# Kernel tuning notes

Measured on AMD Instinct MI355X. Metric: run time of the kernel, lower is better.

The kernel has to match this reference:

```python
import jax, jax.numpy as jnp
import numpy as np

B, S, D = 2, 2048, 2048
H, KVH, DH = 16, 4, 128
WIN = 128
THETA = 10000.0  # local rope (layer_idx=0 -> local/sliding path)


def setup_inputs() -> dict:
    key = jax.random.key(0)
    ks = jax.random.split(key, 5)
    return {
        "x": jax.random.normal(ks[0], (B, S, D), dtype=jnp.float32),
        "Wq": jax.random.normal(ks[1], (H * DH, D), dtype=jnp.float32) * 0.02,
        "Wk": jax.random.normal(ks[2], (KVH * DH, D), dtype=jnp.float32) * 0.02,
        "Wv": jax.random.normal(ks[3], (KVH * DH, D), dtype=jnp.float32) * 0.02,
        "Wo": jax.random.normal(ks[4], (D, H * DH), dtype=jnp.float32) * 0.02,
    }


def _rotate_half(t):
    half = t.shape[-1] // 2
    return jnp.concatenate([-t[..., half:], t[..., :half]], axis=-1)


def _rope_tables(seq_len, head_dim, theta, dtype):
    inv_freq = 1.0 / (theta ** (jnp.arange(0, head_dim, 2, dtype=jnp.float32) / head_dim))
    freqs = jnp.arange(seq_len, dtype=jnp.float32)[:, None] * inv_freq[None, :]  # [S, DH/2]
    # source does repeat_interleave(cos, 2, dim=-1): [S, DH]
    cos = jnp.repeat(jnp.cos(freqs), 2, axis=-1).astype(dtype)
    sin = jnp.repeat(jnp.sin(freqs), 2, axis=-1).astype(dtype)
    return cos[None, :, None, :], sin[None, :, None, :]  # broadcast over [B,S,H,DH]


def reference(x, Wq, Wk, Wv, Wo):
    b, s, _ = x.shape
    q = (x @ Wq.T).reshape(b, s, H, DH)
    k = (x @ Wk.T).reshape(b, s, KVH, DH)
    v = (x @ Wv.T).reshape(b, s, KVH, DH)

    cos, sin = _rope_tables(s, DH, THETA, x.dtype)
    q = q * cos + _rotate_half(q) * sin
    k = k * cos + _rotate_half(k) * sin

    # GQA: repeat_interleave kv heads to n_heads
    groups = H // KVH
    k = jnp.repeat(k, groups, axis=2)
    v = jnp.repeat(v, groups, axis=2)

    q = q.transpose(0, 2, 1, 3)  # [B,H,S,DH]
    k = k.transpose(0, 2, 1, 3)
    v = v.transpose(0, 2, 1, 3)

    scale = DH ** -0.5
    scores = jnp.einsum('bhqd,bhkd->bhqk', q, k) * scale  # [B,H,S,S]

    # faithful local mask from source: q_idx >= k_idx - window_size
    iq = jnp.arange(s)[:, None]
    ik = jnp.arange(s)[None, :]
    mask = iq >= (ik - WIN)  # [S,S]
    scores = jnp.where(mask[None, None, :, :], scores, jnp.float32(-jnp.inf).astype(scores.dtype))

    attn = jax.nn.softmax(scores, axis=-1)
    out = jnp.einsum('bhqk,bhkd->bhqd', attn, v)
    out = out.transpose(0, 2, 1, 3).reshape(b, s, H * DH)
    return out @ Wo.T
```

## Files before the change

### kernel.cpp

```cpp
#include <hip/hip_runtime.h>
#include <hip/hip_bf16.h>

using bf16 = __hip_bfloat16;
typedef __attribute__((ext_vector_type(8))) short short8;
typedef __attribute__((ext_vector_type(4))) float floatx4;

#define AS1 __attribute__((address_space(1)))
#define AS3 __attribute__((address_space(3)))

__device__ __forceinline__ floatx4 mfma16(short8 a, short8 b, floatx4 c) {
  return __builtin_amdgcn_mfma_f32_16x16x32_bf16(a, b, c, 0, 0, 0);
}
__device__ __forceinline__ void gload16(const bf16* g, bf16* l) {
  __builtin_amdgcn_global_load_lds((const AS1 unsigned*)g, (AS3 unsigned*)l, 16, 0, 0);
}

__global__ void cast_bf16_k(const float* __restrict__ src, bf16* __restrict__ dst, int n) {
  int i = (blockIdx.x * 256 + threadIdx.x) * 4;
  if (i >= n) return;
  float4 v = *(const float4*)(src + i);
  bf16 t[4] = {__float2bfloat16(v.x), __float2bfloat16(v.y),
               __float2bfloat16(v.z), __float2bfloat16(v.w)};
  *(ushort4*)(dst + i) = *(const ushort4*)t;
}

template <typename OutT>
__global__ __launch_bounds__(256, 2)
void gemm_bt(const bf16* __restrict__ A, const bf16* __restrict__ B,
             OutT* __restrict__ C, int M, int N, int K) {
  __shared__ alignas(16) bf16 As[128 * 32];
  __shared__ alignas(16) bf16 Bs[128 * 32];
  const int tid = threadIdx.x;
  const int w = tid >> 6, lane = tid & 63, l16 = lane & 15, quad = lane >> 4;
  const int bm = blockIdx.x << 7, bn = blockIdx.y << 7;
  const int wm = (w & 1) << 6, wn = (w >> 1) << 6;

  const int r = tid >> 2, p = tid & 3;
  const int g0 = (p ^ ((r >> 1) & 3)) << 3;
  const int g1 = (p ^ (((r + 64) >> 1) & 3)) << 3;
  const bf16* Ag0 = A + (long)(bm + r) * K + g0;
  const bf16* Ag1 = A + (long)(bm + r + 64) * K + g1;
  const bf16* Bg0 = B + (long)(bn + r) * K + g0;
  const bf16* Bg1 = B + (long)(bn + r + 64) * K + g1;
  bf16* Asw = As + (w << 9);
  bf16* Bsw = Bs + (w << 9);

  floatx4 acc[4][4];
#pragma unroll
  for (int i = 0; i < 4; ++i)
#pragma unroll
    for (int j = 0; j < 4; ++j) acc[i][j] = (floatx4)(0.0f);

  for (int k0 = 0; k0 < K; k0 += 32) {
    gload16(Ag0 + k0, Asw);
    gload16(Ag1 + k0, Asw + 2048);
    gload16(Bg0 + k0, Bsw);
    gload16(Bg1 + k0, Bsw + 2048);
    __syncthreads();
    short8 af[4], bfv[4];
#pragma unroll
    for (int mi = 0; mi < 4; ++mi) {
      int row = wm + (mi << 4) + l16;
      int pos = quad ^ ((row >> 1) & 3);
      af[mi] = *(const short8*)(As + row * 32 + pos * 8);
    }
#pragma unroll
    for (int ni = 0; ni < 4; ++ni) {
      int row = wn + (ni << 4) + l16;
      int pos = quad ^ ((row >> 1) & 3);
      bfv[ni] = *(const short8*)(Bs + row * 32 + pos * 8);
    }
#pragma unroll
    for (int mi = 0; mi < 4; ++mi)
#pragma unroll
      for (int ni = 0; ni < 4; ++ni)
        acc[mi][ni] = mfma16(af[mi], bfv[ni], acc[mi][ni]);
    __syncthreads();
  }

#pragma unroll
  for (int mi = 0; mi < 4; ++mi)
#pragma unroll
    for (int ni = 0; ni < 4; ++ni)
#pragma unroll
      for (int rr = 0; rr < 4; ++rr) {
        int row = bm + wm + (mi << 4) + (quad << 2) + rr;
        int col = bn + wn + (ni << 4) + l16;
        float v = acc[mi][ni][rr];
        if constexpr (sizeof(OutT) == 2)
          C[(long)row * N + col] = __float2bfloat16(v);
        else
          C[(long)row * N + col] = v;
      }
}

__global__ void rope_k(const bf16* __restrict__ qkv, bf16* __restrict__ Q,
                       bf16* __restrict__ Kd) {
  int idx = blockIdx.x * 256 + threadIdx.x;
  int d = idx & 63;
  int rest = idx >> 6;
  int head = rest % 20;
  int token = rest / 20;
  int s = token & 2047;
  int b = token >> 11;
  const float C0 = 0.20762050593046439f;
  float i1 = (float)(d >> 1);
  float inv1 = exp2f(-i1 * C0);
  float inv2 = exp2f(-(i1 + 32.0f) * C0);
  float a1 = (float)s * inv1, a2 = (float)s * inv2;
  float s1, c1, s2, c2;
  sincosf(a1, &s1, &c1);
  sincosf(a2, &s2, &c2);
  if (head < 16) {
    const bf16* p = qkv + (long)token * 3072 + head * 128 + d;
    float xlo = __bfloat162float(p[0]), xhi = __bfloat162float(p[64]);
    const float sc = 0.08838834764831845f * 1.4426950408889634f;
    float olo = (xlo * c1 - xhi * s1) * sc;
    float ohi = (xhi * c2 + xlo * s2) * sc;
    bf16* q = Q + ((long)((b << 4) + head) * 2048 + s) * 128 + d;
    q[0] = __float2bfloat16(olo);
    q[64] = __float2bfloat16(ohi);
  } else {
    int kvh = head - 16;
    const bf16* p = qkv + (long)token * 3072 + 2048 + kvh * 128 + d;
    float xlo = __bfloat162float(p[0]), xhi = __bfloat162float(p[64]);
    float olo = xlo * c1 - xhi * s1;
    float ohi = xhi * c2 + xlo * s2;
    bf16* kk = Kd + ((long)((b << 2) + kvh) * 2048 + s) * 128 + d;
    kk[0] = __float2bfloat16(olo);
    kk[64] = __float2bfloat16(ohi);
  }
}

__global__ void vtrans_k(const bf16* __restrict__ qkv, bf16* __restrict__ Vt) {
  __shared__ bf16 t[32][33];
  int x = threadIdx.x, y = threadIdx.y;
  int s0 = blockIdx.x << 5, d0 = blockIdx.y << 5, bkv = blockIdx.z;
  int b = bkv >> 2, kvh = bkv & 3;
  const bf16* src = qkv + (long)((b << 11) + s0) * 3072 + 2560 + kvh * 128 + d0;
#pragma unroll
  for (int yy = y; yy < 32; yy += 8) t[yy][x] = src[(long)yy * 3072 + x];
  __syncthreads();
  bf16* dst = Vt + (long)((bkv << 7) + d0) * 2048 + s0;
#pragma unroll
  for (int yy = y; yy < 32; yy += 8) dst[(long)yy * 2048 + x] = t[x][yy];
}

__global__ __launch_bounds__(256, 2)
void attn_k(const bf16* __restrict__ Q, const bf16* __restrict__ K,
            const bf16* __restrict__ V, bf16* __restrict__ O) {
  __shared__ alignas(16) bf16 lk[64 * 128];
  __shared__ alignas(16) bf16 lv[128 * 64];
  __shared__ alignas(16) bf16 lpA[4 * 16 * 64];
  __shared__ alignas(16) bf16 lpB[4 * 16 * 64];
  const int tid = threadIdx.x, w = tid >> 6, lane = tid & 63;
  const int l16 = lane & 15, quad = lane >> 4;
  const int bx = blockIdx.x;
  const int qa0 = bx << 6, qb0 = (31 - bx) << 6;
  const int ja_last = bx + 2;
  const int jb_mask = 33 - bx;
  const int jb_last = jb_mask < 31 ? jb_mask : 31;
  const int bh = blockIdx.y, b = bh >> 4, h = bh & 15, kvh = h >> 2;
  const bf16* Qp = Q + (long)bh * 2048 * 128;
  const bf16* Kp = K + (long)((b << 2) + kvh) * 2048 * 128;
  const bf16* Vp = V + (long)((b << 2) + kvh) * 128 * 2048;

  short8 qfA[4], qfB[4];
#pragma unroll
  for (int kc = 0; kc < 4; ++kc) {
    qfA[kc] = *(const short8*)(Qp + (long)(qa0 + (w << 4) + l16) * 128 + kc * 32 + quad * 8);
    qfB[kc] = *(const short8*)(Qp + (long)(qb0 + (w << 4) + l16) * 128 + kc * 32 + quad * 8);
  }

  floatx4 oA[8], oB[8];
#pragma unroll
  for (int i = 0; i < 8; ++i) { oA[i] = (floatx4)(0.0f); oB[i] = (floatx4)(0.0f); }
  float lAcc[4], lBcc[4];
#pragma unroll
  for (int rr = 0; rr < 4; ++rr) { lAcc[rr] = 0.0f; lBcc[rr] = 0.0f; }

  const int sp = (l16 ^ (l16 >> 3)) & 7;
  bf16* pwA = lpA + (w << 10);
  bf16* pwB = lpB + (w << 10);

  auto tile = [&](auto bothc, int k0, bool maskA, bool maskB) {
    constexpr bool BOTH = decltype(bothc)::value;
    floatx4 sA[4], sB[4];
#pragma unroll
    for (int ni = 0; ni < 4; ++ni) {
      sB[ni] = (floatx4)(0.0f);
      if constexpr (BOTH) sA[ni] = (floatx4)(0.0f);
    }
#pragma unroll
    for (int kc = 0; kc < 4; ++kc) {
#pragma unroll
      for (int ni = 0; ni < 4; ++ni) {
        int row = (ni << 4) + l16;
        int g = (kc << 2) + quad;
        int pos = (g & 8) | ((g & 7) ^ (row & 7));
        short8 kf = *(const short8*)(lk + row * 128 + pos * 8);
        sB[ni] = mfma16(qfB[kc], kf, sB[ni]);
        if constexpr (BOTH) sA[ni] = mfma16(qfA[kc], kf, sA[ni]);
      }
    }
    if constexpr (BOTH) {
      if (maskA) {
#pragma unroll
        for (int ni = 0; ni < 4; ++ni) {
          int kg = k0 + (ni << 4) + l16;
#pragma unroll
          for (int rr = 0; rr < 4; ++rr) {
            int qg = qa0 + (w << 4) + (quad << 2) + rr;
            if (kg > qg + 128) sA[ni][rr] = -1e30f;
          }
        }
      }
    }
    if (maskB) {
#pragma unroll
      for (int ni = 0; ni < 4; ++ni) {
        int kg = k0 + (ni << 4) + l16;
#pragma unroll
        for (int rr = 0; rr < 4; ++rr) {
          int qg = qb0 + (w << 4) + (quad << 2) + rr;
          if (kg > qg + 128) sB[ni][rr] = -1e30f;
        }
      }
    }
#pragma unroll
    for (int ni = 0; ni < 4; ++ni) {
      int cc = (ni << 4) + l16;
      int g = cc >> 3;
#pragma unroll
      for (int rr = 0; rr < 4; ++rr) {
        int row = (quad << 2) + rr;
        int srow = (row ^ (row >> 3)) & 7;
        int addr = row * 64 + ((g ^ srow) << 3) + (cc & 7);
        float pB = exp2f(sB[ni][rr]);
        lBcc[rr] += pB;
        pwB[addr] = __float2bfloat16(pB);
        if constexpr (BOTH) {
          float pA = exp2f(sA[ni][rr]);
          lAcc[rr] += pA;
          pwA[addr] = __float2bfloat16(pA);
        }
      }
    }
#pragma unroll
    for (int kc = 0; kc < 2; ++kc) {
      int g = (kc << 2) + quad;
      short8 pfB = *(const short8*)(pwB + l16 * 64 + ((g ^ sp) << 3));
      short8 pfA;
      if constexpr (BOTH) pfA = *(const short8*)(pwA + l16 * 64 + ((g ^ sp) << 3));
#pragma unroll
      for (int ni = 0; ni < 8; ++ni) {
        int vrow = (ni << 4) + l16;
        int vpos = g ^ (vrow & 7);
        short8 vf = *(const short8*)(lv + vrow * 64 + (vpos << 3));
        oB[ni] = mfma16(pfB, vf, oB[ni]);
        if constexpr (BOTH) oA[ni] = mfma16(pfA, vf, oA[ni]);
      }
    }
  };

  for (int j = 0; j <= jb_last; ++j) {
    const int k0 = j << 6;
#pragma unroll
    for (int i = 0; i < 4; ++i) {
      int c = i * 256 + tid;
      int row = c >> 4, pos = c & 15;
      int grp = (pos & 8) | ((pos & 7) ^ (row & 7));
      gload16(Kp + (long)(k0 + row) * 128 + grp * 8, lk + (i * 256 + (w << 6)) * 8);
    }
#pragma unroll
    for (int i = 0; i < 4; ++i) {
      int c = i * 256 + tid;
      int row = c >> 3, grp = (c & 7) ^ (row & 7);
      gload16(Vp + (long)row * 2048 + k0 + grp * 8, lv + (i * 256 + (w << 6)) * 8);
    }
    __syncthreads();
    if (j <= ja_last)
      tile(std::integral_constant<bool, true>{}, k0, j == ja_last, j == jb_mask);
    else
      tile(std::integral_constant<bool, false>{}, k0, false, j == jb_mask);
    __syncthreads();
  }

#pragma unroll
  for (int off = 1; off <= 8; off <<= 1)
#pragma unroll
    for (int rr = 0; rr < 4; ++rr) {
      lAcc[rr] += __shfl_xor(lAcc[rr], off, 64);
      lBcc[rr] += __shfl_xor(lBcc[rr], off, 64);
    }
  float rlA[4], rlB[4];
#pragma unroll
  for (int rr = 0; rr < 4; ++rr) { rlA[rr] = 1.0f / lAcc[rr]; rlB[rr] = 1.0f / lBcc[rr]; }

  bf16* OpA = O + ((long)(b << 11) + qa0 + (w << 4)) * 2048 + (h << 7);
  bf16* OpB = O + ((long)(b << 11) + qb0 + (w << 4)) * 2048 + (h << 7);
#pragma unroll
  for (int ni = 0; ni < 8; ++ni)
#pragma unroll
    for (int rr = 0; rr < 4; ++rr) {
      int row = (quad << 2) + rr;
      int col = (ni << 4) + l16;
      OpA[(long)row * 2048 + col] = __float2bfloat16(oA[ni][rr] * rlA[rr]);
      OpB[(long)row * 2048 + col] = __float2bfloat16(oB[ni][rr] * rlB[rr]);
    }
}

extern "C" void kernel_launch(void* const* d_in, const int* in_sizes, int n_in,
                              void* d_out, int out_size, void* d_ws, size_t ws_size,
                              hipStream_t stream) {
  (void)in_sizes; (void)n_in; (void)out_size; (void)ws_size;
  const float* x  = (const float*)d_in[0];
  const float* Wq = (const float*)d_in[1];
  const float* Wk = (const float*)d_in[2];
  const float* Wv = (const float*)d_in[3];
  const float* Wo = (const float*)d_in[4];
  char* ws = (char*)d_ws;
  bf16* xb   = (bf16*)(ws);
  bf16* wqkv = (bf16*)(ws + 16777216);
  bf16* wo_b = (bf16*)(ws + 29360128);
  bf16* qkv  = (bf16*)(ws + 37748736);
  bf16* Qr   = (bf16*)(ws + 62914560);
  bf16* Kr   = (bf16*)(ws + 79691776);
  bf16* Vt   = (bf16*)(ws + 83886080);
  bf16* Ob   = xb;
  float* out = (float*)d_out;

  cast_bf16_k<<<8192, 256, 0, stream>>>(x, xb, 8388608);
  cast_bf16_k<<<4096, 256, 0, stream>>>(Wq, wqkv, 4194304);
  cast_bf16_k<<<1024, 256, 0, stream>>>(Wk, wqkv + 2048 * 2048, 1048576);
  cast_bf16_k<<<1024, 256, 0, stream>>>(Wv, wqkv + 2560 * 2048, 1048576);
  cast_bf16_k<<<4096, 256, 0, stream>>>(Wo, wo_b, 4194304);

  gemm_bt<bf16><<<dim3(32, 24), 256, 0, stream>>>(xb, wqkv, qkv, 4096, 3072, 2048);
  rope_k<<<20480, 256, 0, stream>>>(qkv, Qr, Kr);
  vtrans_k<<<dim3(64, 4, 8), dim3(32, 8), 0, stream>>>(qkv, Vt);
  attn_k<<<dim3(16, 32), 256, 0, stream>>>(Qr, Kr, Vt, Ob);
  gemm_bt<float><<<dim3(32, 16), 256, 0, stream>>>(Ob, wo_b, out, 4096, 2048, 2048);
}
```

Before: 335.7 us.

## Use 128-key attention tiles with transposed S and merge cast launches

```diff
diff --git a/kernel.cpp b/kernel.cpp
--- a/kernel.cpp
+++ b/kernel.cpp
@@ -15,9 +15,20 @@
   __builtin_amdgcn_global_load_lds((const AS1 unsigned*)g, (AS3 unsigned*)l, 16, 0, 0);
 }
 
-__global__ void cast_bf16_k(const float* __restrict__ src, bf16* __restrict__ dst, int n) {
-  int i = (blockIdx.x * 256 + threadIdx.x) * 4;
-  if (i >= n) return;
+__global__ void cast_all_k(const float* __restrict__ x, const float* __restrict__ Wq,
+                           const float* __restrict__ Wk, const float* __restrict__ Wv,
+                           const float* __restrict__ Wo, bf16* __restrict__ xb,
+                           bf16* __restrict__ wqkv, bf16* __restrict__ wo_b) {
+  int blk = blockIdx.x;
+  const float* src;
+  bf16* dst;
+  int off;
+  if (blk < 8192)       { src = x;  dst = xb;                 off = blk; }
+  else if (blk < 12288) { src = Wq; dst = wqkv;               off = blk - 8192; }
+  else if (blk < 13312) { src = Wk; dst = wqkv + 2048 * 2048; off = blk - 12288; }
+  else if (blk < 14336) { src = Wv; dst = wqkv + 2560 * 2048; off = blk - 13312; }
+  else                  { src = Wo; dst = wo_b;               off = blk - 14336; }
+  int i = (off * 256 + threadIdx.x) * 4;
   float4 v = *(const float4*)(src + i);
   bf16 t[4] = {__float2bfloat16(v.x), __float2bfloat16(v.y),
                __float2bfloat16(v.z), __float2bfloat16(v.w)};
@@ -149,17 +160,18 @@
 __global__ __launch_bounds__(256, 2)
 void attn_k(const bf16* __restrict__ Q, const bf16* __restrict__ K,
             const bf16* __restrict__ V, bf16* __restrict__ O) {
-  __shared__ alignas(16) bf16 lk[64 * 128];
-  __shared__ alignas(16) bf16 lv[128 * 64];
+  __shared__ alignas(16) bf16 lk[128 * 128];
+  __shared__ alignas(16) bf16 lv[128 * 128];
   __shared__ alignas(16) bf16 lpA[4 * 16 * 64];
   __shared__ alignas(16) bf16 lpB[4 * 16 * 64];
   const int tid = threadIdx.x, w = tid >> 6, lane = tid & 63;
   const int l16 = lane & 15, quad = lane >> 4;
   const int bx = blockIdx.x;
   const int qa0 = bx << 6, qb0 = (31 - bx) << 6;
-  const int ja_last = bx + 2;
-  const int jb_mask = 33 - bx;
-  const int jb_last = jb_mask < 31 ? jb_mask : 31;
+  const int nkA = (bx >> 1) + 2;
+  int nkBt = ((31 - bx) >> 1) + 2;
+  const int nkB = nkBt < 16 ? nkBt : 16;
+  const int jmA = (bx >> 1) + 1, jmB = ((31 - bx) >> 1) + 1;
   const int bh = blockIdx.y, b = bh >> 4, h = bh & 15, kvh = h >> 2;
   const bf16* Qp = Q + (long)bh * 2048 * 128;
   const bf16* Kp = K + (long)((b << 2) + kvh) * 2048 * 128;
@@ -175,138 +187,143 @@
   floatx4 oA[8], oB[8];
 #pragma unroll
   for (int i = 0; i < 8; ++i) { oA[i] = (floatx4)(0.0f); oB[i] = (floatx4)(0.0f); }
-  float lAcc[4], lBcc[4];
-#pragma unroll
-  for (int rr = 0; rr < 4; ++rr) { lAcc[rr] = 0.0f; lBcc[rr] = 0.0f; }
-
-  const int sp = (l16 ^ (l16 >> 3)) & 7;
+  float lA = 0.0f, lB = 0.0f;
+
   bf16* pwA = lpA + (w << 10);
   bf16* pwB = lpB + (w << 10);
+  const int sw = l16 & 7;
 
   auto tile = [&](auto bothc, int k0, bool maskA, bool maskB) {
     constexpr bool BOTH = decltype(bothc)::value;
-    floatx4 sA[4], sB[4];
-#pragma unroll
-    for (int ni = 0; ni < 4; ++ni) {
-      sB[ni] = (floatx4)(0.0f);
-      if constexpr (BOTH) sA[ni] = (floatx4)(0.0f);
+    floatx4 sA[8], sB[8];
+#pragma unroll
+    for (int kt = 0; kt < 8; ++kt) {
+      sB[kt] = (floatx4)(0.0f);
+      if constexpr (BOTH) sA[kt] = (floatx4)(0.0f);
     }
 #pragma unroll
     for (int kc = 0; kc < 4; ++kc) {
 #pragma unroll
-      for (int ni = 0; ni < 4; ++ni) {
-        int row = (ni << 4) + l16;
+      for (int kt = 0; kt < 8; ++kt) {
+        int row = (kt << 4) + l16;
         int g = (kc << 2) + quad;
         int pos = (g & 8) | ((g & 7) ^ (row & 7));
         short8 kf = *(const short8*)(lk + row * 128 + pos * 8);
-        sB[ni] = mfma16(qfB[kc], kf, sB[ni]);
-        if constexpr (BOTH) sA[ni] = mfma16(qfA[kc], kf, sA[ni]);
-      }
+        sB[kt] = mfma16(kf, qfB[kc], sB[kt]);
+        if constexpr (BOTH) sA[kt] = mfma16(kf, qfA[kc], sA[kt]);
+      }
+    }
+    if (maskB) {
+      int qg = qb0 + (w << 4) + l16 + 128;
+#pragma unroll
+      for (int kt = 0; kt < 8; ++kt)
+#pragma unroll
+        for (int rr = 0; rr < 4; ++rr) {
+          int kg = k0 + (kt << 4) + (quad << 2) + rr;
+          if (kg > qg) sB[kt][rr] = -1e30f;
+        }
     }
     if constexpr (BOTH) {
       if (maskA) {
-#pragma unroll
-        for (int ni = 0; ni < 4; ++ni) {
-          int kg = k0 + (ni << 4) + l16;
+        int qg = qa0 + (w << 4) + l16 + 128;
+#pragma unroll
+        for (int kt = 0; kt < 8; ++kt)
 #pragma unroll
           for (int rr = 0; rr < 4; ++rr) {
-            int qg = qa0 + (w << 4) + (quad << 2) + rr;
-            if (kg > qg + 128) sA[ni][rr] = -1e30f;
+            int kg = k0 + (kt << 4) + (quad << 2) + rr;
+            if (kg > qg) sA[kt][rr] = -1e30f;
           }
+      }
+    }
+#pragma unroll
+    for (int hh = 0; hh < 2; ++hh) {
+#pragma unroll
+      for (int t = 0; t < 4; ++t) {
+        int kt = (hh << 2) + t;
+        int slot = (t << 2) + quad;
+        int sl = ((((slot >> 1) ^ sw) << 1) | (quad & 1)) << 2;
+        {
+          float p0 = exp2f(sB[kt][0]), p1 = exp2f(sB[kt][1]);
+          float p2 = exp2f(sB[kt][2]), p3 = exp2f(sB[kt][3]);
+          lB += (p0 + p1) + (p2 + p3);
+          bf16 tb[4] = {__float2bfloat16(p0), __float2bfloat16(p1),
+                        __float2bfloat16(p2), __float2bfloat16(p3)};
+          *(ushort4*)(pwB + (l16 << 6) + sl) = *(const ushort4*)tb;
         }
-      }
-    }
-    if (maskB) {
-#pragma unroll
-      for (int ni = 0; ni < 4; ++ni) {
-        int kg = k0 + (ni << 4) + l16;
-#pragma unroll
-        for (int rr = 0; rr < 4; ++rr) {
-          int qg = qb0 + (w << 4) + (quad << 2) + rr;
-          if (kg > qg + 128) sB[ni][rr] = -1e30f;
+        if constexpr (BOTH) {
+          float p0 = exp2f(sA[kt][0]), p1 = exp2f(sA[kt][1]);
+          float p2 = exp2f(sA[kt][2]), p3 = exp2f(sA[kt][3]);
+          lA += (p0 + p1) + (p2 + p3);
+          bf16 ta[4] = {__float2bfloat16(p0), __float2bfloat16(p1),
+                        __float2bfloat16(p2), __float2bfloat16(p3)};
+          *(ushort4*)(pwA + (l16 << 6) + sl) = *(const ushort4*)ta;
         }
       }
-    }
-#pragma unroll
-    for (int ni = 0; ni < 4; ++ni) {
-      int cc = (ni << 4) + l16;
-      int g = cc >> 3;
-#pragma unroll
-      for (int rr = 0; rr < 4; ++rr) {
-        int row = (quad << 2) + rr;
-        int srow = (row ^ (row >> 3)) & 7;
-        int addr = row * 64 + ((g ^ srow) << 3) + (cc & 7);
-        float pB = exp2f(sB[ni][rr]);
-        lBcc[rr] += pB;
-        pwB[addr] = __float2bfloat16(pB);
-        if constexpr (BOTH) {
-          float pA = exp2f(sA[ni][rr]);
-          lAcc[rr] += pA;
-          pwA[addr] = __float2bfloat16(pA);
+#pragma unroll
+      for (int kcl = 0; kcl < 2; ++kcl) {
+        int pp = ((kcl << 2) + quad) ^ sw;
+        short8 pfB = *(const short8*)(pwB + (l16 << 6) + (pp << 3));
+        short8 pfA;
+        if constexpr (BOTH) pfA = *(const short8*)(pwA + (l16 << 6) + (pp << 3));
+        int kcg = (hh << 1) + kcl;
+#pragma unroll
+        for (int nd = 0; nd < 8; ++nd) {
+          int vrow = (nd << 4) + l16;
+          int g = (kcg << 2) + quad;
+          int pos = (g & 8) | ((g & 7) ^ (vrow & 7));
+          short8 vf = *(const short8*)(lv + vrow * 128 + pos * 8);
+          oB[nd] = mfma16(pfB, vf, oB[nd]);
+          if constexpr (BOTH) oA[nd] = mfma16(pfA, vf, oA[nd]);
         }
       }
     }
-#pragma unroll
-    for (int kc = 0; kc < 2; ++kc) {
-      int g = (kc << 2) + quad;
-      short8 pfB = *(const short8*)(pwB + l16 * 64 + ((g ^ sp) << 3));
-      short8 pfA;
-      if constexpr (BOTH) pfA = *(const short8*)(pwA + l16 * 64 + ((g ^ sp) << 3));
-#pragma unroll
-      for (int ni = 0; ni < 8; ++ni) {
-        int vrow = (ni << 4) + l16;
-        int vpos = g ^ (vrow & 7);
-        short8 vf = *(const short8*)(lv + vrow * 64 + (vpos << 3));
-        oB[ni] = mfma16(pfB, vf, oB[ni]);
-        if constexpr (BOTH) oA[ni] = mfma16(pfA, vf, oA[ni]);
-      }
-    }
   };
 
-  for (int j = 0; j <= jb_last; ++j) {
-    const int k0 = j << 6;
-#pragma unroll
-    for (int i = 0; i < 4; ++i) {
+  for (int j = 0; j < nkB; ++j) {
+    const int k0 = j << 7;
+#pragma unroll
+    for (int i = 0; i < 8; ++i) {
       int c = i * 256 + tid;
       int row = c >> 4, pos = c & 15;
-      int grp = (pos & 8) | ((pos & 7) ^ (row & 7));
-      gload16(Kp + (long)(k0 + row) * 128 + grp * 8, lk + (i * 256 + (w << 6)) * 8);
-    }
-#pragma unroll
-    for (int i = 0; i < 4; ++i) {
+      int g = (pos & 8) | ((pos & 7) ^ (row & 7));
+      gload16(Kp + (long)(k0 + row) * 128 + g * 8, lk + (i * 256 + (w << 6)) * 8);
+    }
+#pragma unroll
+    for (int i = 0; i < 8; ++i) {
       int c = i * 256 + tid;
-      int row = c >> 3, grp = (c & 7) ^ (row & 7);
-      gload16(Vp + (long)row * 2048 + k0 + grp * 8, lv + (i * 256 + (w << 6)) * 8);
+      int row = c >> 4, pos = c & 15;
+      int g = (pos & 8) | ((pos & 7) ^ (row & 7));
+      gload16(Vp + (long)row * 2048 + k0 + g * 8, lv + (i * 256 + (w << 6)) * 8);
     }
     __syncthreads();
-    if (j <= ja_last)
-      tile(std::integral_constant<bool, true>{}, k0, j == ja_last, j == jb_mask);
+    if (j < nkA)
+      tile(std::integral_constant<bool, true>{}, k0, j == jmA, j == jmB);
     else
-      tile(std::integral_constant<bool, false>{}, k0, false, j == jb_mask);
+      tile(std::integral_constant<bool, false>{}, k0, false, j == jmB);
     __syncthreads();
   }
 
-#pragma unroll
-  for (int off = 1; off <= 8; off <<= 1)
-#pragma unroll
-    for (int rr = 0; rr < 4; ++rr) {
-      lAcc[rr] += __shfl_xor(lAcc[rr], off, 64);
-      lBcc[rr] += __shfl_xor(lBcc[rr], off, 64);
-    }
+  lA += __shfl_xor(lA, 16, 64); lA += __shfl_xor(lA, 32, 64);
+  lB += __shfl_xor(lB, 16, 64); lB += __shfl_xor(lB, 32, 64);
+  float liA = 1.0f / lA, liB = 1.0f / lB;
   float rlA[4], rlB[4];
 #pragma unroll
-  for (int rr = 0; rr < 4; ++rr) { rlA[rr] = 1.0f / lAcc[rr]; rlB[rr] = 1.0f / lBcc[rr]; }
+  for (int rr = 0; rr < 4; ++rr) {
+    int src = (quad << 2) + rr;
+    rlA[rr] = __shfl(liA, src, 64);
+    rlB[rr] = __shfl(liB, src, 64);
+  }
 
   bf16* OpA = O + ((long)(b << 11) + qa0 + (w << 4)) * 2048 + (h << 7);
   bf16* OpB = O + ((long)(b << 11) + qb0 + (w << 4)) * 2048 + (h << 7);
 #pragma unroll
-  for (int ni = 0; ni < 8; ++ni)
+  for (int nd = 0; nd < 8; ++nd)
 #pragma unroll
     for (int rr = 0; rr < 4; ++rr) {
       int row = (quad << 2) + rr;
-      int col = (ni << 4) + l16;
-      OpA[(long)row * 2048 + col] = __float2bfloat16(oA[ni][rr] * rlA[rr]);
-      OpB[(long)row * 2048 + col] = __float2bfloat16(oB[ni][rr] * rlB[rr]);
+      int col = (nd << 4) + l16;
+      OpA[(long)row * 2048 + col] = __float2bfloat16(oA[nd][rr] * rlA[rr]);
+      OpB[(long)row * 2048 + col] = __float2bfloat16(oB[nd][rr] * rlB[rr]);
     }
 }
 
@@ -330,11 +347,7 @@
   bf16* Ob   = xb;
   float* out = (float*)d_out;
 
-  cast_bf16_k<<<8192, 256, 0, stream>>>(x, xb, 8388608);
-  cast_bf16_k<<<4096, 256, 0, stream>>>(Wq, wqkv, 4194304);
-  cast_bf16_k<<<1024, 256, 0, stream>>>(Wk, wqkv + 2048 * 2048, 1048576);
-  cast_bf16_k<<<1024, 256, 0, stream>>>(Wv, wqkv + 2560 * 2048, 1048576);
-  cast_bf16_k<<<4096, 256, 0, stream>>>(Wo, wo_b, 4194304);
+  cast_all_k<<<18432, 256, 0, stream>>>(x, Wq, Wk, Wv, Wo, xb, wqkv, wo_b);
 
   gemm_bt<bf16><<<dim3(32, 24), 256, 0, stream>>>(xb, wqkv, qkv, 4096, 3072, 2048);
   rope_k<<<20480, 256, 0, stream>>>(qkv, Qr, Kr);
```

After: 311.3 us. 7.3% less time.
